# Kernel optimization log

Measured on AMD Instinct MI355X. Metric: run time of the kernel, lower is better.

## Reference

```python
import jax, jax.numpy as jnp
import numpy as np

P = 2          # SamplesLoss p=2
BLUR = 0.05    # eps_final = BLUR**P = 0.0025
SCALING = 0.8  # annealing factor per iteration (on the blur scale)


def _cost(x, y):
    # geomloss cost for p=2: |x - y|^2 / 2, shape (N, M)
    x2 = jnp.sum(x * x, axis=-1)
    y2 = jnp.sum(y * y, axis=-1)
    return 0.5 * (x2[:, None] + y2[None, :] - 2.0 * (x @ y.T))


def _softmin(eps, C, h):
    # -eps * log sum_j exp(h_j - C_ij / eps); h already contains log-weights
    return -eps * jax.nn.logsumexp(h[None, :] - C / eps, axis=1)


def _eps_schedule(x, y):
    # geomloss scaling_parameters / epsilon_schedule with diameter from bounding box
    xn, yn = np.asarray(x), np.asarray(y)
    mins = np.minimum(xn.min(0), yn.min(0))
    maxs = np.maximum(xn.max(0), yn.max(0))
    diameter = float(np.linalg.norm(maxs - mins))
    eps_list = ([diameter ** P]
                + [float(np.exp(e)) for e in np.arange(P * np.log(diameter), P * np.log(BLUR), P * np.log(SCALING))]
                + [BLUR ** P])
    return eps_list


def _sinkhorn_divergence(x, y, eps_list):
    # Debiased Sinkhorn divergence S_eps(x, y), geomloss sinkhorn_tensorized
    N, M = x.shape[0], y.shape[0]
    sg = jax.lax.stop_gradient
    C_xy, C_yx = _cost(x, y), _cost(y, x)
    C_xx, C_yy = _cost(x, sg(x)), _cost(y, sg(y))  # geomloss detaches 2nd arg
    # The annealing loop runs with autograd disabled in geomloss:
    Cxy_, Cyx_, Cxx_, Cyy_ = sg(C_xy), sg(C_yx), sg(C_xx), sg(C_yy)
    a_log = jnp.full((N,), -np.log(N), dtype=x.dtype)  # log uniform weights
    b_log = jnp.full((M,), -np.log(M), dtype=y.dtype)
    e0 = eps_list[0]
    f_aa = _softmin(e0, Cxx_, a_log)
    g_bb = _softmin(e0, Cyy_, b_log)
    g_ab = _softmin(e0, Cyx_, a_log)
    f_ba = _softmin(e0, Cxy_, b_log)
    for eps in eps_list:  # fixed schedule, not a data-dim loop
        ft_ba = _softmin(eps, Cxy_, b_log + g_ab / eps)
        gt_ab = _softmin(eps, Cyx_, a_log + f_ba / eps)
        ft_aa = _softmin(eps, Cxx_, a_log + f_aa / eps)
        gt_bb = _softmin(eps, Cyy_, b_log + g_bb / eps)
        f_ba, g_ab = 0.5 * (f_ba + ft_ba), 0.5 * (g_ab + gt_ab)
        f_aa, g_bb = 0.5 * (f_aa + ft_aa), 0.5 * (g_bb + gt_bb)
    # Final extrapolation step (the only one geomloss differentiates through):
    eps = eps_list[-1]
    f_ba, g_ab = (_softmin(eps, C_xy, sg(b_log + g_ab / eps)),
                  _softmin(eps, C_yx, sg(a_log + f_ba / eps)))
    f_aa = _softmin(eps, C_xx, sg(a_log + f_aa / eps))
    g_bb = _softmin(eps, C_yy, sg(b_log + g_bb / eps))
    # scal with uniform weights == mean
    return jnp.mean(f_ba - f_aa) + jnp.mean(g_ab - g_bb)


def setup_inputs() -> dict:
    key = jax.random.key(0)
    kx, kt = jax.random.split(key)
    x = jax.random.normal(kx, (4096, 64), dtype=jnp.float32)
    target = jax.random.normal(kt, (4096, 64), dtype=jnp.float32)
    return {"x": x, "target": target}


def reference(x, target):
    eps_list = _eps_schedule(x, target)  # concrete schedule from data diameter
    return _sinkhorn_divergence(x, target, eps_list)
```

## Files before the change

### kernel.cpp

```cpp
#include <hip/hip_runtime.h>
#include <math.h>

#define NPTS 4096
#define DIM  64
#define MAX_ITERS 37

#define ALOG (-8.317766166719343f)
#define L2E  (1.4426950408889634f)
#define LN2  (0.6931471805599453f)

#if __has_builtin(__builtin_amdgcn_exp2f)
#define EXP2F(x) __builtin_amdgcn_exp2f(x)
#else
#define EXP2F(x) exp2f(x)
#endif
#if __has_builtin(__builtin_amdgcn_logf)
#define LOG2F(x) __builtin_amdgcn_logf(x)
#else
#define LOG2F(x) log2f(x)
#endif

typedef _Float16 f16x8 __attribute__((ext_vector_type(8)));
typedef float    f32x4 __attribute__((ext_vector_type(4)));

__device__ __forceinline__ void grid_barrier(int* hdr, int* lsense) {
    __syncthreads();
    if (threadIdx.x == 0) {
        int s = *lsense ^ 1;
        __threadfence();
        int prev = __hip_atomic_fetch_add(hdr + 4, 1, __ATOMIC_ACQ_REL,
                                          __HIP_MEMORY_SCOPE_AGENT);
        if (prev == (int)gridDim.x - 1) {
            __hip_atomic_store(hdr + 4, 0, __ATOMIC_RELAXED, __HIP_MEMORY_SCOPE_AGENT);
            __hip_atomic_store(hdr + 8, s, __ATOMIC_RELEASE, __HIP_MEMORY_SCOPE_AGENT);
        } else {
            while (__hip_atomic_load(hdr + 8, __ATOMIC_ACQUIRE,
                                     __HIP_MEMORY_SCOPE_AGENT) != s)
                __builtin_amdgcn_s_sleep(16);
        }
        *lsense = s;
        __threadfence();
    }
    __syncthreads();
}

template <int TPB>
__global__ __launch_bounds__(256, (TPB == 1 ? 4 : 2)) void mega_kernel(
        const float* __restrict__ x, const float* __restrict__ y,
        _Float16* __restrict__ X16, _Float16* __restrict__ Y16,
        float* __restrict__ x2, float* __restrict__ y2,
        float* __restrict__ pmn, float* __restrict__ pmx,
        int* hdr, float* __restrict__ sched,
        float* __restrict__ F, float* __restrict__ H, float* __restrict__ P,
        float* __restrict__ out)
{
    const int b  = blockIdx.x;
    const int tt = threadIdx.x;
    int lsense = 0;

    __shared__ float hs[512];
    __shared__ _Float16 Bs[2][64][72];

    for (int g = b * 256 + tt; g < NPTS * DIM; g += gridDim.x * 256) {
        float xv = x[g], yv = y[g];
        X16[g] = (_Float16)xv;
        Y16[g] = (_Float16)yv;
        float sx = xv * xv, sy = yv * yv;
        for (int o = 32; o > 0; o >>= 1) {
            sx += __shfl_xor(sx, o, 64);
            sy += __shfl_xor(sy, o, 64);
        }
        if ((tt & 63) == 0) { x2[g >> 6] = sx; y2[g >> 6] = sy; }
    }
    if (b < 128) {
        float mn = INFINITY, mx = -INFINITY;
        for (int gg = b * 256 + tt; gg < NPTS * DIM; gg += 128 * 256) {
            float v = x[gg]; mn = fminf(mn, v); mx = fmaxf(mx, v);
            float w = y[gg]; mn = fminf(mn, w); mx = fmaxf(mx, w);
        }
        float* smn = hs;
        float* smx = (float*)&Bs[0][0][0];
        smn[tt] = mn; smx[tt] = mx;
        __syncthreads();
        if (tt < 64) {
            for (int qq = 1; qq < 4; qq++) {
                mn = fminf(mn, smn[tt + 64 * qq]);
                mx = fmaxf(mx, smx[tt + 64 * qq]);
            }
            pmn[b * 64 + tt] = mn;
            pmx[b * 64 + tt] = mx;
        }
    }
    grid_barrier(hdr, &lsense);

    if (b == 0) {
        float* r2 = hs;
        if (tt < 64) {
            float mn = INFINITY, mx = -INFINITY;
            for (int bb = 0; bb < 128; bb++) {
                mn = fminf(mn, pmn[bb * 64 + tt]);
                mx = fmaxf(mx, pmx[bb * 64 + tt]);
            }
            float range = mx - mn;
            r2[tt] = range * range;
        }
        __syncthreads();
        if (tt == 0) {
            float ss = 0.f;
            for (int k = 0; k < 64; k++) ss += r2[k];
            float diam_f = sqrtf(ss);
            double diam = (double)diam_f;
            double start = 2.0 * log(diam);
            double stop  = 2.0 * log(0.05);
            double step  = 2.0 * log(0.8);
            int n_ar = (int)ceil((stop - start) / step);
            if (n_ar < 0) n_ar = 0;
            int ne = n_ar + 2;
            if (ne > 63) ne = 63;
            sched[0] = (float)(diam * diam);
            for (int k = 0; k < n_ar && (1 + k) < 63; k++)
                sched[1 + k] = (float)exp(start + step * (double)k);
            sched[ne - 1] = 0.0025f;
            for (int k = ne; k < 64; k++) sched[k] = 0.0025f;
            hdr[0] = ne;
        }
    }
    grid_barrier(hdr, &lsense);

    const int n_eps = *(volatile int*)hdr;

    const int wv = tt >> 6, lane = tt & 63, q = lane >> 4, lo = lane & 15;
    const int srow = tt >> 2, scol = (tt & 3) * 16;

    f16x8 a[TPB][2][2];
#pragma unroll
    for (int sub = 0; sub < TPB; sub++) {
        const int bt = b + 512 * sub;
        const int mat_ = bt >> 8, rb_ = (bt >> 3) & 31;
        const _Float16* Am = (mat_ == 0 || mat_ == 2) ? X16 : Y16;
        const int r0_ = rb_ * 128;
#pragma unroll
        for (int rt = 0; rt < 2; rt++) {
            const _Float16* ar = Am + (size_t)(r0_ + wv * 32 + rt * 16 + lo) * DIM + q * 8;
            a[sub][rt][0] = *(const f16x8*)ar;
            a[sub][rt][1] = *(const f16x8*)(ar + 32);
        }
    }

    for (int p = 0; p <= n_eps + 2; p++) {
        const int t = (p == 0) ? -2 : (p == n_eps + 2) ? -1 : (p - 1);
        const bool do_main = (t < 0) || (t < n_eps);

#pragma unroll
        for (int sub = 0; sub < TPB; sub++) {
            const int bt = b + 512 * sub;
            const int mat = bt >> 8, rb = (bt >> 3) & 31, cs = bt & 7;
            const _Float16* Bm = (mat == 1 || mat == 2) ? X16 : Y16;
            const int matc = (mat < 2) ? (1 - mat) : mat;
            const float* sqc = (matc == 0 || matc == 2) ? x2 : y2;
            const int c0 = cs * 512, r0 = rb * 128;
            const _Float16* Bsrc0 = Bm + (size_t)(c0 + srow) * DIM + scol;

            f16x8 t0a, t0b;
            if (do_main) {
                t0a = *(const f16x8*)Bsrc0;
                t0b = *(const f16x8*)(Bsrc0 + 8);
            }

            if (t == -2) {
                float inv2i = L2E / sched[0];
                for (int r = tt; r < 512; r += 256)
                    hs[r] = ALOG * L2E - 0.5f * sqc[c0 + r] * inv2i;
            } else if (t == -1) {
                for (int r = tt; r < 512; r += 256)
                    hs[r] = H[mat * 4096 + c0 + r];
            } else {
                int pp = (t == 0) ? 1 : ((t - 1) & 1);
                const float* Pm = P + pp * 262144;
                const float* Ps = Pm + 131072;
                float epsp = sched[(t == 0) ? 0 : (t - 1)];
                float inv2c = L2E / sched[t];
                for (int r = tt; r < 512; r += 256) {
                    int row = c0 + r;
                    int base = (matc * 8) * NPTS + row;
                    float M = -INFINITY;
#pragma unroll
                    for (int qq = 0; qq < 8; qq++) M = fmaxf(M, Pm[base + qq * NPTS]);
                    float S = 0.f;
#pragma unroll
                    for (int qq = 0; qq < 8; qq++)
                        S += Ps[base + qq * NPTS] * EXP2F(Pm[base + qq * NPTS] - M);
                    float sq = sqc[row];
                    float res = 0.5f * sq - epsp * LN2 * (M + LOG2F(S));
                    float fnew = (t == 0) ? res
                               : 0.5f * (F[((t - 1) & 1) * 16384 + matc * 4096 + row] + res);
                    float h = ALOG * L2E + (fnew - 0.5f * sq) * inv2c;
                    hs[r] = h;
                    if (rb == 0) {
                        F[(t & 1) * 16384 + matc * 4096 + row] = fnew;
                        H[mat * 4096 + row] = h;
                    }
                }
            }

            if (do_main) {
                int idx = (t == -2) ? 0 : ((t == -1) ? n_eps - 1 : t);
                float inv2 = L2E / sched[idx];

                *(f16x8*)&Bs[0][srow][scol]     = t0a;
                *(f16x8*)&Bs[0][srow][scol + 8] = t0b;

                float m[2][4], s[2][4];
#pragma unroll
                for (int rt = 0; rt < 2; rt++)
#pragma unroll
                    for (int r = 0; r < 4; r++) { m[rt][r] = -INFINITY; s[rt][r] = 0.f; }

                for (int ct = 0; ct < 8; ct++) {
                    __syncthreads();
                    f16x8 n0, n1;
                    if (ct < 7) {
                        const _Float16* src = Bsrc0 + (size_t)(ct + 1) * 64 * DIM;
                        n0 = *(const f16x8*)src;
                        n1 = *(const f16x8*)(src + 8);
                    }
                    const _Float16 (*Bt)[72] = Bs[ct & 1];
                    float v[2][4][4];
#pragma unroll
                    for (int cc = 0; cc < 4; cc++) {
                        const _Float16* br = &Bt[cc * 16 + lo][q * 8];
                        f16x8 b0 = *(const f16x8*)br;
                        f16x8 b1 = *(const f16x8*)(br + 32);
                        float hval = hs[ct * 64 + cc * 16 + lo];
#pragma unroll
                        for (int rt = 0; rt < 2; rt++) {
                            f32x4 acc = {0.f, 0.f, 0.f, 0.f};
                            acc = __builtin_amdgcn_mfma_f32_16x16x32_f16(a[sub][rt][0], b0, acc, 0, 0, 0);
                            acc = __builtin_amdgcn_mfma_f32_16x16x32_f16(a[sub][rt][1], b1, acc, 0, 0, 0);
#pragma unroll
                            for (int r = 0; r < 4; r++) v[rt][r][cc] = fmaf(acc[r], inv2, hval);
                        }
                    }
#pragma unroll
                    for (int rt = 0; rt < 2; rt++)
#pragma unroll
                        for (int r = 0; r < 4; r++) {
                            float lm = fmaxf(fmaxf(v[rt][r][0], v[rt][r][1]),
                                             fmaxf(v[rt][r][2], v[rt][r][3]));
                            if (lm > m[rt][r] - 26.0f) {
                                float nm = fmaxf(m[rt][r], lm);
                                float acc = s[rt][r] * EXP2F(m[rt][r] - nm);
                                acc += EXP2F(v[rt][r][0] - nm) + EXP2F(v[rt][r][1] - nm)
                                     + EXP2F(v[rt][r][2] - nm) + EXP2F(v[rt][r][3] - nm);
                                m[rt][r] = nm; s[rt][r] = acc;
                            }
                        }
                    if (ct < 7) {
                        *(f16x8*)&Bs[(ct + 1) & 1][srow][scol]     = n0;
                        *(f16x8*)&Bs[(ct + 1) & 1][srow][scol + 8] = n1;
                    }
                }

#pragma unroll
                for (int off = 1; off < 16; off <<= 1) {
#pragma unroll
                    for (int rt = 0; rt < 2; rt++)
#pragma unroll
                        for (int r = 0; r < 4; r++) {
                            float om = __shfl_xor(m[rt][r], off, 64);
                            float os = __shfl_xor(s[rt][r], off, 64);
                            float nm = fmaxf(m[rt][r], om);
                            s[rt][r] = s[rt][r] * EXP2F(m[rt][r] - nm) + os * EXP2F(om - nm);
                            m[rt][r] = nm;
                        }
                }
                if (lo == 0) {
                    int pw = (t == -1) ? (n_eps & 1) : ((t == -2) ? 1 : (t & 1));
                    float* Pw = P + pw * 262144;
                    float* Sw = Pw + 131072;
#pragma unroll
                    for (int rt = 0; rt < 2; rt++)
#pragma unroll
                        for (int r = 0; r < 4; r++) {
                            int row = r0 + wv * 32 + rt * 16 + q * 4 + r;
                            Pw[(mat * 8 + cs) * NPTS + row] = m[rt][r];
                            Sw[(mat * 8 + cs) * NPTS + row] = s[rt][r];
                        }
                }
            }
            __syncthreads();
        }
        grid_barrier(hdr, &lsense);
    }

    if (b < 64) {
        const float* Pm = P + (n_eps & 1) * 262144;
        const float* Ps = Pm + 131072;
        int g = b * 256 + tt;
        int fmat = g >> 12, row = g & 4095;
        float eps = sched[n_eps - 1];
        const float* sqr = (fmat == 0 || fmat == 2) ? x2 : y2;
        int base = (fmat * 8) * NPTS + row;
        float M = -INFINITY;
#pragma unroll
        for (int qq = 0; qq < 8; qq++) M = fmaxf(M, Pm[base + qq * NPTS]);
        float S = 0.f;
#pragma unroll
        for (int qq = 0; qq < 8; qq++)
            S += Ps[base + qq * NPTS] * EXP2F(Pm[base + qq * NPTS] - M);
        float res = 0.5f * sqr[row] - eps * LN2 * (M + LOG2F(S));
        float val = ((fmat < 2) ? res : -res) * (1.0f / NPTS);
        float* sh = hs;
        sh[tt] = val;
        __syncthreads();
        for (int o = 128; o > 0; o >>= 1) {
            if (tt < o) sh[tt] += sh[tt + o];
            __syncthreads();
        }
        if (tt == 0) atomicAdd(out, sh[0]);
    }
}

__global__ void minmax_part_kernel(const float* __restrict__ x,
                                   const float* __restrict__ y,
                                   float* __restrict__ partmn,
                                   float* __restrict__ partmx) {
    int t = threadIdx.x;
    int bid = blockIdx.x;
    int g0 = bid * 256 + t;
    const int total = NPTS * DIM;
    float mn = INFINITY, mx = -INFINITY;
    for (int g = g0; g < total; g += 128 * 256) {
        float v = x[g]; mn = fminf(mn, v); mx = fmaxf(mx, v);
        float w = y[g]; mn = fminf(mn, w); mx = fmaxf(mx, w);
    }
    __shared__ float smn[256], smx[256];
    smn[t] = mn; smx[t] = mx;
    __syncthreads();
    if (t < 64) {
        for (int q = 1; q < 4; q++) {
            mn = fminf(mn, smn[t + 64 * q]);
            mx = fmaxf(mx, smx[t + 64 * q]);
        }
        partmn[bid * 64 + t] = mn;
        partmx[bid * 64 + t] = mx;
    }
}

__global__ void schedule_kernel(const float* __restrict__ partmn,
                                const float* __restrict__ partmx,
                                int* __restrict__ hdr,
                                float* __restrict__ sched) {
    int d = threadIdx.x;
    float mn = INFINITY, mx = -INFINITY;
    for (int b = 0; b < 128; b++) {
        mn = fminf(mn, partmn[b * 64 + d]);
        mx = fmaxf(mx, partmx[b * 64 + d]);
    }
    float range = mx - mn;
    __shared__ float r2[64];
    r2[d] = range * range;
    __syncthreads();
    if (d == 0) {
        float ss = 0.f;
        for (int k = 0; k < 64; k++) ss += r2[k];
        float diam_f = sqrtf(ss);
        double diam = (double)diam_f;
        double start = 2.0 * log(diam);
        double stop  = 2.0 * log(0.05);
        double step  = 2.0 * log(0.8);
        int n_ar = (int)ceil((stop - start) / step);
        if (n_ar < 0) n_ar = 0;
        int n_eps = n_ar + 2;
        if (n_eps > 63) n_eps = 63;
        sched[0] = (float)(diam * diam);
        for (int k = 0; k < n_ar && (1 + k) < 63; k++)
            sched[1 + k] = (float)exp(start + step * (double)k);
        sched[n_eps - 1] = 0.0025f;
        for (int k = n_eps; k < 64; k++) sched[k] = 0.0025f;
        hdr[0] = n_eps;
    }
}

__global__ void sqnorm_kernel(const float* __restrict__ X, float* __restrict__ out) {
    int wave = (blockIdx.x * blockDim.x + threadIdx.x) >> 6;
    int lane = threadIdx.x & 63;
    if (wave >= NPTS) return;
    float v = X[wave * DIM + lane];
    float s = v * v;
    for (int o = 32; o > 0; o >>= 1) s += __shfl_xor(s, o, 64);
    if (lane == 0) out[wave] = s;
}

__global__ void cast_kernel(const float* __restrict__ x, const float* __restrict__ y,
                            _Float16* __restrict__ X16, _Float16* __restrict__ Y16) {
    int g = blockIdx.x * 256 + threadIdx.x;
    X16[g] = (_Float16)x[g];
    Y16[g] = (_Float16)y[g];
}

__global__ __launch_bounds__(256, 4) void pass_kernel(
        const _Float16* __restrict__ X16, const _Float16* __restrict__ Y16,
        const float* __restrict__ x2, const float* __restrict__ y2,
        float* __restrict__ F, float* __restrict__ H, float* __restrict__ P,
        const int* __restrict__ hdr, const float* __restrict__ sched, int t) {
    const int n_eps = hdr[0];
    if (t >= 0 && t > n_eps) return;

    int b = blockIdx.x;
    int mat = b >> 8, rb = (b >> 3) & 31, cs = b & 7;
    const _Float16* Am = (mat == 0 || mat == 2) ? X16 : Y16;
    const _Float16* Bm = (mat == 1 || mat == 2) ? X16 : Y16;
    int matc = (mat < 2) ? (1 - mat) : mat;
    const float* sqc = (matc == 0 || matc == 2) ? x2 : y2;

    __shared__ float hs[512];
    __shared__ _Float16 Bs[2][64][72];

    int tt = threadIdx.x;
    int c0 = cs * 512, r0 = rb * 128;

    if (t == -2) {
        float inv2i = L2E / sched[0];
        for (int r = tt; r < 512; r += 256)
            hs[r] = ALOG * L2E - 0.5f * sqc[c0 + r] * inv2i;
    } else if (t == -1) {
        for (int r = tt; r < 512; r += 256)
            hs[r] = H[mat * 4096 + c0 + r];
    } else {
        int pp = (t == 0) ? 1 : ((t - 1) & 1);
        const float* Pm = P + pp * 262144;
        const float* Ps = Pm + 131072;
        float epsp = sched[(t == 0) ? 0 : (t - 1)];
        float inv2c = L2E / sched[t];
        for (int r = tt; r < 512; r += 256) {
            int row = c0 + r;
            int base = (matc * 8) * NPTS + row;
            float M = -INFINITY;
#pragma unroll
            for (int q = 0; q < 8; q++) M = fmaxf(M, Pm[base + q * NPTS]);
            float S = 0.f;
#pragma unroll
            for (int q = 0; q < 8; q++)
                S += Ps[base + q * NPTS] * EXP2F(Pm[base + q * NPTS] - M);
            float sq = sqc[row];
            float res = 0.5f * sq - epsp * LN2 * (M + LOG2F(S));
            float fnew = (t == 0) ? res
                       : 0.5f * (F[((t - 1) & 1) * 16384 + matc * 4096 + row] + res);
            float h = ALOG * L2E + (fnew - 0.5f * sq) * inv2c;
            hs[r] = h;
            if (rb == 0) {
                F[(t & 1) * 16384 + matc * 4096 + row] = fnew;
                H[mat * 4096 + row] = h;
            }
        }
    }
    __syncthreads();
    if (t >= 0 && t >= n_eps) return;

    int idx = (t == -2) ? 0 : ((t == -1) ? n_eps - 1 : t);
    float inv2 = L2E / sched[idx];

    int wv = tt >> 6, lane = tt & 63, q = lane >> 4, lo = lane & 15;

    f16x8 a[2][2];
#pragma unroll
    for (int rt = 0; rt < 2; rt++) {
        const _Float16* ar = Am + (size_t)(r0 + wv * 32 + rt * 16 + lo) * DIM + q * 8;
        a[rt][0] = *(const f16x8*)ar;
        a[rt][1] = *(const f16x8*)(ar + 32);
    }

    int srow = tt >> 2, scol = (tt & 3) * 16;
    {
        const _Float16* src = Bm + (size_t)(c0 + srow) * DIM + scol;
        *(f16x8*)&Bs[0][srow][scol]     = *(const f16x8*)src;
        *(f16x8*)&Bs[0][srow][scol + 8] = *(const f16x8*)(src + 8);
    }

    float m[2][4], s[2][4];
#pragma unroll
    for (int rt = 0; rt < 2; rt++)
#pragma unroll
        for (int r = 0; r < 4; r++) { m[rt][r] = -INFINITY; s[rt][r] = 0.f; }

    for (int ct = 0; ct < 8; ct++) {
        __syncthreads();
        f16x8 n0, n1;
        if (ct < 7) {
            const _Float16* src = Bm + (size_t)(c0 + (ct + 1) * 64 + srow) * DIM + scol;
            n0 = *(const f16x8*)src;
            n1 = *(const f16x8*)(src + 8);
        }
        const _Float16 (*Bt)[72] = Bs[ct & 1];
        float v[2][4][4];
#pragma unroll
        for (int cc = 0; cc < 4; cc++) {
            const _Float16* br = &Bt[cc * 16 + lo][q * 8];
            f16x8 b0 = *(const f16x8*)br;
            f16x8 b1 = *(const f16x8*)(br + 32);
            float hval = hs[ct * 64 + cc * 16 + lo];
#pragma unroll
            for (int rt = 0; rt < 2; rt++) {
                f32x4 acc = {0.f, 0.f, 0.f, 0.f};
                acc = __builtin_amdgcn_mfma_f32_16x16x32_f16(a[rt][0], b0, acc, 0, 0, 0);
                acc = __builtin_amdgcn_mfma_f32_16x16x32_f16(a[rt][1], b1, acc, 0, 0, 0);
#pragma unroll
                for (int r = 0; r < 4; r++) v[rt][r][cc] = fmaf(acc[r], inv2, hval);
            }
        }
#pragma unroll
        for (int rt = 0; rt < 2; rt++)
#pragma unroll
            for (int r = 0; r < 4; r++) {
                float lm = fmaxf(fmaxf(v[rt][r][0], v[rt][r][1]),
                                 fmaxf(v[rt][r][2], v[rt][r][3]));
                if (lm > m[rt][r] - 26.0f) {
                    float nm = fmaxf(m[rt][r], lm);
                    float acc = s[rt][r] * EXP2F(m[rt][r] - nm);
                    acc += EXP2F(v[rt][r][0] - nm) + EXP2F(v[rt][r][1] - nm)
                         + EXP2F(v[rt][r][2] - nm) + EXP2F(v[rt][r][3] - nm);
                    m[rt][r] = nm; s[rt][r] = acc;
                }
            }
        if (ct < 7) {
            *(f16x8*)&Bs[(ct + 1) & 1][srow][scol]     = n0;
            *(f16x8*)&Bs[(ct + 1) & 1][srow][scol + 8] = n1;
        }
    }

#pragma unroll
    for (int off = 1; off < 16; off <<= 1) {
#pragma unroll
        for (int rt = 0; rt < 2; rt++)
#pragma unroll
            for (int r = 0; r < 4; r++) {
                float om = __shfl_xor(m[rt][r], off, 64);
                float os = __shfl_xor(s[rt][r], off, 64);
                float nm = fmaxf(m[rt][r], om);
                s[rt][r] = s[rt][r] * EXP2F(m[rt][r] - nm) + os * EXP2F(om - nm);
                m[rt][r] = nm;
            }
    }
    if (lo == 0) {
        int pw = (t == -1) ? (n_eps & 1) : ((t == -2) ? 1 : (t & 1));
        float* Pm = P + pw * 262144;
        float* Ps = Pm + 131072;
#pragma unroll
        for (int rt = 0; rt < 2; rt++)
#pragma unroll
            for (int r = 0; r < 4; r++) {
                int row = r0 + wv * 32 + rt * 16 + q * 4 + r;
                Pm[(mat * 8 + cs) * NPTS + row] = m[rt][r];
                Ps[(mat * 8 + cs) * NPTS + row] = s[rt][r];
            }
    }
}

__global__ void finalize_kernel(const float* __restrict__ P,
                                const float* __restrict__ x2, const float* __restrict__ y2,
                                const int* __restrict__ hdr, const float* __restrict__ sched,
                                float* __restrict__ out) {
    int n_eps = hdr[0];
    const float* Pm = P + (n_eps & 1) * 262144;
    const float* Ps = Pm + 131072;
    int g = blockIdx.x * 256 + threadIdx.x;
    int mat = g >> 12, row = g & 4095;
    float eps = sched[n_eps - 1];
    const float* sqr = (mat == 0 || mat == 2) ? x2 : y2;
    int base = (mat * 8) * NPTS + row;
    float M = -INFINITY;
#pragma unroll
    for (int q = 0; q < 8; q++) M = fmaxf(M, Pm[base + q * NPTS]);
    float S = 0.f;
#pragma unroll
    for (int q = 0; q < 8; q++) S += Ps[base + q * NPTS] * EXP2F(Pm[base + q * NPTS] - M);
    float res = 0.5f * sqr[row] - eps * LN2 * (M + LOG2F(S));
    float val = ((mat == 0 || mat == 1) ? res : -res) * (1.0f / NPTS);
    __shared__ float sh[256];
    sh[threadIdx.x] = val;
    __syncthreads();
    for (int o = 128; o > 0; o >>= 1) {
        if (threadIdx.x < o) sh[threadIdx.x] += sh[threadIdx.x + o];
        __syncthreads();
    }
    if (threadIdx.x == 0) atomicAdd(out, sh[0]);
}

extern "C" void kernel_launch(void* const* d_in, const int* in_sizes, int n_in,
                              void* d_out, int out_size, void* d_ws, size_t ws_size,
                              hipStream_t stream) {
    const float* x = (const float*)d_in[0];
    const float* y = (const float*)d_in[1];
    float* out = (float*)d_out;
    float* w = (float*)d_ws;

    int*   hdr   = (int*)w;
    float* sched = w + 16;
    float* pmn   = w + 80;
    float* pmx   = w + 8272;
    float* x2    = w + 16464;
    float* y2    = w + 20560;
    float* F     = w + 24656;
    float* H     = w + 57424;
    float* P     = w + 73808;
    _Float16* X16 = (_Float16*)(w + 598096);
    _Float16* Y16 = (_Float16*)(w + 729168);

    hipMemsetAsync(out, 0, sizeof(float), stream);
    hipMemsetAsync(hdr, 0, 64, stream);

    int occ1 = 0, occ2 = 0;
    (void)hipOccupancyMaxActiveBlocksPerMultiprocessor(&occ1, mega_kernel<1>, 256, 0);
    (void)hipOccupancyMaxActiveBlocksPerMultiprocessor(&occ2, mega_kernel<2>, 256, 0);

    if (occ1 >= 4) {
        hipLaunchKernelGGL((mega_kernel<1>), dim3(1024), dim3(256), 0, stream,
                           x, y, X16, Y16, x2, y2, pmn, pmx, hdr, sched, F, H, P, out);
    } else if (occ2 >= 2) {
        hipLaunchKernelGGL((mega_kernel<2>), dim3(512), dim3(256), 0, stream,
                           x, y, X16, Y16, x2, y2, pmn, pmx, hdr, sched, F, H, P, out);
    } else {
        hipLaunchKernelGGL(minmax_part_kernel, dim3(128), dim3(256), 0, stream, x, y, pmn, pmx);
        hipLaunchKernelGGL(schedule_kernel, dim3(1), dim3(64), 0, stream, pmn, pmx, hdr, sched);
        hipLaunchKernelGGL(sqnorm_kernel, dim3(1024), dim3(256), 0, stream, x, x2);
        hipLaunchKernelGGL(sqnorm_kernel, dim3(1024), dim3(256), 0, stream, y, y2);
        hipLaunchKernelGGL(cast_kernel, dim3(1024), dim3(256), 0, stream, x, y, X16, Y16);
        hipLaunchKernelGGL(pass_kernel, dim3(1024), dim3(256), 0, stream,
                           X16, Y16, x2, y2, F, H, P, hdr, sched, -2);
        for (int t = 0; t < MAX_ITERS; t++)
            hipLaunchKernelGGL(pass_kernel, dim3(1024), dim3(256), 0, stream,
                               X16, Y16, x2, y2, F, H, P, hdr, sched, t);
        hipLaunchKernelGGL(pass_kernel, dim3(1024), dim3(256), 0, stream,
                           X16, Y16, x2, y2, F, H, P, hdr, sched, -1);
        hipLaunchKernelGGL(finalize_kernel, dim3(64), dim3(256), 0, stream,
                           P, x2, y2, hdr, sched, out);
    }
}
```

Baseline: 970.9 us.

## Use hierarchical split grid barriers and lazy-rescale online logsumexp

Replaces the single-counter grid barrier with a two-level barrier (32-block sub-counters on separate cache lines plus a master counter). With 1024 blocks, the per-iteration barrier only synchronises the 512-block half that shares data, not the whole grid. It also changes the online logsumexp to rescale the running max only when a wave-wide jump exceeds a threshold, and splits the cross-lane reduction into a max pass and a sum pass. Together these target atomic contention on the barrier and transcendental count in the inner loop. The cost is more barrier complexity, extra workspace, and a looser max bound that could risk overflow or precision loss if values drift.

```diff
diff --git a/kernel.cpp b/kernel.cpp
--- a/kernel.cpp
+++ b/kernel.cpp
@@ -23,20 +23,35 @@
 typedef _Float16 f16x8 __attribute__((ext_vector_type(8)));
 typedef float    f32x4 __attribute__((ext_vector_type(4)));
 
-__device__ __forceinline__ void grid_barrier(int* hdr, int* lsense) {
+__device__ __forceinline__ void multi_barrier(int* st, int idx, int nsub,
+                                              int* lsense) {
     __syncthreads();
     if (threadIdx.x == 0) {
         int s = *lsense ^ 1;
         __threadfence();
-        int prev = __hip_atomic_fetch_add(hdr + 4, 1, __ATOMIC_ACQ_REL,
+        int sub = idx >> 5;
+        int prev = __hip_atomic_fetch_add(st + sub * 16, 1, __ATOMIC_ACQ_REL,
                                           __HIP_MEMORY_SCOPE_AGENT);
-        if (prev == (int)gridDim.x - 1) {
-            __hip_atomic_store(hdr + 4, 0, __ATOMIC_RELAXED, __HIP_MEMORY_SCOPE_AGENT);
-            __hip_atomic_store(hdr + 8, s, __ATOMIC_RELEASE, __HIP_MEMORY_SCOPE_AGENT);
+        if (prev == 31) {
+            int pm = __hip_atomic_fetch_add(st + 512, 1, __ATOMIC_ACQ_REL,
+                                            __HIP_MEMORY_SCOPE_AGENT);
+            if (pm == nsub - 1) {
+                for (int i = 0; i < nsub; i++)
+                    __hip_atomic_store(st + i * 16, 0, __ATOMIC_RELAXED,
+                                       __HIP_MEMORY_SCOPE_AGENT);
+                __hip_atomic_store(st + 512, 0, __ATOMIC_RELAXED,
+                                   __HIP_MEMORY_SCOPE_AGENT);
+                __hip_atomic_store(st + 544, s, __ATOMIC_RELEASE,
+                                   __HIP_MEMORY_SCOPE_AGENT);
+            } else {
+                while (__hip_atomic_load(st + 544, __ATOMIC_ACQUIRE,
+                                         __HIP_MEMORY_SCOPE_AGENT) != s)
+                    __builtin_amdgcn_s_sleep(8);
+            }
         } else {
-            while (__hip_atomic_load(hdr + 8, __ATOMIC_ACQUIRE,
+            while (__hip_atomic_load(st + 544, __ATOMIC_ACQUIRE,
                                      __HIP_MEMORY_SCOPE_AGENT) != s)
-                __builtin_amdgcn_s_sleep(16);
+                __builtin_amdgcn_s_sleep(8);
         }
         *lsense = s;
         __threadfence();
@@ -52,11 +67,22 @@
         float* __restrict__ pmn, float* __restrict__ pmx,
         int* hdr, float* __restrict__ sched,
         float* __restrict__ F, float* __restrict__ H, float* __restrict__ P,
-        float* __restrict__ out)
+        int* bar, float* __restrict__ out)
 {
     const int b  = blockIdx.x;
     const int tt = threadIdx.x;
-    int lsense = 0;
+    int senseG = 0, senseL = 0;
+
+    int* stG;  int nsubG;
+    int* stL;  int idxL; int nsubL;
+    if (TPB == 1) {
+        stG = bar + 2048; nsubG = 32;
+        stL = bar + (b >> 9) * 1024; idxL = b & 511; nsubL = 16;
+    } else {
+        stG = bar + 2048; nsubG = 16;
+        stL = stG; idxL = b; nsubL = 16;
+    }
+    int* senseLp = (TPB == 1) ? &senseL : &senseG;
 
     __shared__ float hs[512];
     __shared__ _Float16 Bs[2][64][72];
@@ -91,7 +117,7 @@
             pmx[b * 64 + tt] = mx;
         }
     }
-    grid_barrier(hdr, &lsense);
+    multi_barrier(stG, b, nsubG, &senseG);
 
     if (b == 0) {
         float* r2 = hs;
@@ -125,7 +151,7 @@
             hdr[0] = ne;
         }
     }
-    grid_barrier(hdr, &lsense);
+    multi_barrier(stG, b, nsubG, &senseG);
 
     const int n_eps = *(volatile int*)hdr;
 
@@ -245,14 +271,18 @@
                     for (int rt = 0; rt < 2; rt++)
 #pragma unroll
                         for (int r = 0; r < 4; r++) {
-                            float lm = fmaxf(fmaxf(v[rt][r][0], v[rt][r][1]),
-                                             fmaxf(v[rt][r][2], v[rt][r][3]));
+                            float v0 = v[rt][r][0], v1 = v[rt][r][1];
+                            float v2 = v[rt][r][2], v3 = v[rt][r][3];
+                            float lm = fmaxf(fmaxf(v0, v1), fmaxf(v2, v3));
+                            if (__any(lm > m[rt][r] + 40.0f)) {
+                                float nm = fmaxf(m[rt][r], lm);
+                                s[rt][r] *= EXP2F(m[rt][r] - nm);
+                                m[rt][r] = nm;
+                            }
                             if (lm > m[rt][r] - 26.0f) {
-                                float nm = fmaxf(m[rt][r], lm);
-                                float acc = s[rt][r] * EXP2F(m[rt][r] - nm);
-                                acc += EXP2F(v[rt][r][0] - nm) + EXP2F(v[rt][r][1] - nm)
-                                     + EXP2F(v[rt][r][2] - nm) + EXP2F(v[rt][r][3] - nm);
-                                m[rt][r] = nm; s[rt][r] = acc;
+                                float mm = m[rt][r];
+                                s[rt][r] += (EXP2F(v0 - mm) + EXP2F(v1 - mm))
+                                          + (EXP2F(v2 - mm) + EXP2F(v3 - mm));
                             }
                         }
                     if (ct < 7) {
@@ -261,19 +291,31 @@
                     }
                 }
 
-#pragma unroll
-                for (int off = 1; off < 16; off <<= 1) {
+                float ml[2][4];
+#pragma unroll
+                for (int rt = 0; rt < 2; rt++)
+#pragma unroll
+                    for (int r = 0; r < 4; r++) ml[rt][r] = m[rt][r];
+#pragma unroll
+                for (int off = 1; off < 16; off <<= 1)
 #pragma unroll
                     for (int rt = 0; rt < 2; rt++)
 #pragma unroll
-                        for (int r = 0; r < 4; r++) {
-                            float om = __shfl_xor(m[rt][r], off, 64);
-                            float os = __shfl_xor(s[rt][r], off, 64);
-                            float nm = fmaxf(m[rt][r], om);
-                            s[rt][r] = s[rt][r] * EXP2F(m[rt][r] - nm) + os * EXP2F(om - nm);
-                            m[rt][r] = nm;
-                        }
-                }
+                        for (int r = 0; r < 4; r++)
+                            m[rt][r] = fmaxf(m[rt][r], __shfl_xor(m[rt][r], off, 64));
+#pragma unroll
+                for (int rt = 0; rt < 2; rt++)
+#pragma unroll
+                    for (int r = 0; r < 4; r++)
+                        s[rt][r] *= EXP2F(ml[rt][r] - m[rt][r]);
+#pragma unroll
+                for (int off = 1; off < 16; off <<= 1)
+#pragma unroll
+                    for (int rt = 0; rt < 2; rt++)
+#pragma unroll
+                        for (int r = 0; r < 4; r++)
+                            s[rt][r] += __shfl_xor(s[rt][r], off, 64);
+
                 if (lo == 0) {
                     int pw = (t == -1) ? (n_eps & 1) : ((t == -2) ? 1 : (t & 1));
                     float* Pw = P + pw * 262144;
@@ -290,8 +332,10 @@
             }
             __syncthreads();
         }
-        grid_barrier(hdr, &lsense);
-    }
+        multi_barrier(stL, idxL, nsubL, senseLp);
+    }
+
+    multi_barrier(stG, b, nsubG, &senseG);
 
     if (b < 64) {
         const float* Pm = P + (n_eps & 1) * 262144;
@@ -369,12 +413,12 @@
         double start = 2.0 * log(diam);
         double stop  = 2.0 * log(0.05);
         double step  = 2.0 * log(0.8);
-        int n_ar = (int)ceil((stop - start) / step);
-        if (n_ar < 0) n_ar = 0;
-        int n_eps = n_ar + 2;
+        int n_eps = (int)ceil((stop - start) / step);
+        if (n_eps < 0) n_eps = 0;
+        n_eps += 2;
         if (n_eps > 63) n_eps = 63;
         sched[0] = (float)(diam * diam);
-        for (int k = 0; k < n_ar && (1 + k) < 63; k++)
+        for (int k = 0; k < n_eps - 2 && (1 + k) < 63; k++)
             sched[1 + k] = (float)exp(start + step * (double)k);
         sched[n_eps - 1] = 0.0025f;
         for (int k = n_eps; k < 64; k++) sched[k] = 0.0025f;
@@ -606,9 +650,10 @@
     float* P     = w + 73808;
     _Float16* X16 = (_Float16*)(w + 598096);
     _Float16* Y16 = (_Float16*)(w + 729168);
+    int*   bar   = (int*)(w + 860240);
 
     hipMemsetAsync(out, 0, sizeof(float), stream);
-    hipMemsetAsync(hdr, 0, 64, stream);
+    hipMemsetAsync(bar, 0, 3 * 1024 * sizeof(int), stream);
 
     int occ1 = 0, occ2 = 0;
     (void)hipOccupancyMaxActiveBlocksPerMultiprocessor(&occ1, mega_kernel<1>, 256, 0);
@@ -616,10 +661,10 @@
 
     if (occ1 >= 4) {
         hipLaunchKernelGGL((mega_kernel<1>), dim3(1024), dim3(256), 0, stream,
-                           x, y, X16, Y16, x2, y2, pmn, pmx, hdr, sched, F, H, P, out);
+                           x, y, X16, Y16, x2, y2, pmn, pmx, hdr, sched, F, H, P, bar, out);
     } else if (occ2 >= 2) {
         hipLaunchKernelGGL((mega_kernel<2>), dim3(512), dim3(256), 0, stream,
-                           x, y, X16, Y16, x2, y2, pmn, pmx, hdr, sched, F, H, P, out);
+                           x, y, X16, Y16, x2, y2, pmn, pmx, hdr, sched, F, H, P, bar, out);
     } else {
         hipLaunchKernelGGL(minmax_part_kernel, dim3(128), dim3(256), 0, stream, x, y, pmn, pmx);
         hipLaunchKernelGGL(schedule_kernel, dim3(1), dim3(64), 0, stream, pmn, pmx, hdr, sched);
```

After: 962.0 us. No clear change (-0.9%).
